# Kernel tuning notes

Measured on AMD Instinct MI355X. Metric: run time of the kernel, lower is better.

The kernel has to match this reference:

```python
import jax, jax.numpy as jnp
import numpy as np

N = 200000
F_IN = 128
F_OUT = 128
NBRS = 4  # NEIGHBORHOOD_SIZE - 1 (self counted separately)


def setup_inputs() -> dict:
    key = jax.random.key(0)
    k1, k2, k3, k4, k5 = jax.random.split(key, 5)
    features = jax.random.normal(k1, (N, F_IN), dtype=jnp.float32)
    prev_features = jax.random.normal(k2, (N, F_IN), dtype=jnp.float32)
    neighbor_idx = jax.random.randint(k3, (N, NBRS), 0, N, dtype=jnp.int32)
    # nn.Linear(5*in, out): weight [out, 5*in], bias [out]
    W = jax.random.normal(k4, (F_OUT, 5 * F_IN), dtype=jnp.float32) * 0.02
    b = jax.random.normal(k5, (F_OUT,), dtype=jnp.float32) * 0.02
    return {"features": features, "prev_features": prev_features,
            "neighbor_idx": neighbor_idx, "W": W, "b": b}


def reference(features, prev_features, neighbor_idx, W, b):
    # gather neighbor prev_features: [N, 4, F_IN] -> [N, 4*F_IN]
    nbr = prev_features[neighbor_idx].reshape(N, NBRS * F_IN)
    # concat self features first (matches torch loop order): [N, 5*F_IN]
    gathered = jnp.concatenate([features, nbr], axis=1)
    # linear: y = gathered @ W^T + b -> [N, F_OUT]
    new_features = jnp.einsum('nk,ok->no', gathered, W) + b
    # module sets tet.features = new_features and prev_features = features;
    # both end up equal to new_features.
    return new_features
```

## Files before the change

kernel.cpp:

```cpp
#include <hip/hip_runtime.h>


#define N_PTS  200000
#define F_INN  128
#define K_TOT  640
#define NCHUNK 40
#define NCT    4

typedef __attribute__((ext_vector_type(8)))  short bf16x8;
typedef __attribute__((ext_vector_type(16))) float f32x16;
typedef __attribute__((ext_vector_type(8)))  float f32x8;

union Frag { bf16x8 v; unsigned int u[4]; };

__device__ __forceinline__ unsigned int bf_rne_bits(float f) {
    unsigned int u = __builtin_bit_cast(unsigned int, f);
    return (u + 0x7FFFu + ((u >> 16) & 1u)) & 0xFFFF0000u;
}

__device__ __forceinline__ void split8_rne(const f32x8 a, bf16x8& hi, bf16x8& lo) {
    Frag H, L;
#pragma unroll
    for (int p = 0; p < 4; ++p) {
        float f0 = a[2 * p], f1 = a[2 * p + 1];
        unsigned int h0 = bf_rne_bits(f0), h1 = bf_rne_bits(f1);
        float r0 = f0 - __builtin_bit_cast(float, h0);
        float r1 = f1 - __builtin_bit_cast(float, h1);
        unsigned int l0 = bf_rne_bits(r0), l1 = bf_rne_bits(r1);
        H.u[p] = (h0 >> 16) | h1;
        L.u[p] = (l0 >> 16) | l1;
    }
    hi = H.v; lo = L.v;
}

__device__ __forceinline__ void split8_trunc(const f32x8 a, bf16x8& hi, bf16x8& lo) {
    Frag H, L;
#pragma unroll
    for (int p = 0; p < 4; ++p) {
        float f0 = a[2 * p], f1 = a[2 * p + 1];
        unsigned int u0 = __builtin_bit_cast(unsigned int, f0);
        unsigned int u1 = __builtin_bit_cast(unsigned int, f1);
        unsigned int h0 = u0 & 0xFFFF0000u, h1 = u1 & 0xFFFF0000u;
        float r0 = f0 - __builtin_bit_cast(float, h0);
        float r1 = f1 - __builtin_bit_cast(float, h1);
        unsigned int l0 = __builtin_bit_cast(unsigned int, r0);
        unsigned int l1 = __builtin_bit_cast(unsigned int, r1);
        H.u[p] = (h0 >> 16) | h1;
        L.u[p] = (l0 >> 16) | (l1 & 0xFFFF0000u);
    }
    hi = H.v; lo = L.v;
}

__global__ void build_wf(const float* __restrict__ W,
                         bf16x8* __restrict__ wf_hi,
                         bf16x8* __restrict__ wf_lo) {
    int tid = blockIdx.x * blockDim.x + threadIdx.x;
    int lane = tid & 63;
    int ct   = (tid >> 6) & 3;
    int t    = tid >> 8;
    if (t >= NCHUNK) return;
    int c = ct * 32 + (lane & 31);
    int k = t * 16 + (lane >> 5) * 8;
    f32x8 w = *(const f32x8*)(W + (size_t)c * K_TOT + k);
    bf16x8 h, l;
    split8_rne(w, h, l);
    wf_hi[tid] = h;
    wf_lo[tid] = l;
}

__global__ __launch_bounds__(256, 2)
void mcconv(const float* __restrict__ feat, const float* __restrict__ prev,
            const int* __restrict__ nbr, const float* __restrict__ bias,
            const bf16x8* __restrict__ wf_hi, const bf16x8* __restrict__ wf_lo,
            float* __restrict__ out) {
    const int lane = threadIdx.x & 63;
    const int wave = threadIdx.x >> 6;
    const int g    = lane >> 5;
    const int r31  = lane & 31;
    const int n0   = blockIdx.x * 256 + wave * 64;

    int nA = n0 + r31;
    int nB = n0 + 32 + r31;
    int nAc = nA < N_PTS ? nA : N_PTS - 1;
    int nBc = nB < N_PTS ? nB : N_PTS - 1;

    const int4 iA = *(const int4*)(nbr + 4 * (size_t)nAc);
    const int4 iB = *(const int4*)(nbr + 4 * (size_t)nBc);

    f32x16 acc[2][NCT];
#pragma unroll
    for (int m = 0; m < 2; ++m)
#pragma unroll
        for (int c = 0; c < NCT; ++c)
#pragma unroll
            for (int i = 0; i < 16; ++i) acc[m][c][i] = 0.0f;

    for (int s = 0; s < 5; ++s) {
        const float* pA;
        const float* pB;
        if (s == 0)      { pA = feat + (size_t)nAc * F_INN;  pB = feat + (size_t)nBc * F_INN; }
        else if (s == 1) { pA = prev + (size_t)iA.x * F_INN; pB = prev + (size_t)iB.x * F_INN; }
        else if (s == 2) { pA = prev + (size_t)iA.y * F_INN; pB = prev + (size_t)iB.y * F_INN; }
        else if (s == 3) { pA = prev + (size_t)iA.z * F_INN; pB = prev + (size_t)iB.z * F_INN; }
        else             { pA = prev + (size_t)iA.w * F_INN; pB = prev + (size_t)iB.w * F_INN; }

#pragma unroll
        for (int cc = 0; cc < 8; ++cc) {
            const int t = s * 8 + cc;
            f32x8 a0 = *(const f32x8*)(pA + cc * 16 + g * 8);
            f32x8 a1 = *(const f32x8*)(pB + cc * 16 + g * 8);

            bf16x8 bh[NCT], bl[NCT];
#pragma unroll
            for (int ct = 0; ct < NCT; ++ct) {
                int fi = (t * 4 + ct) * 64 + lane;
                bh[ct] = wf_hi[fi];
                bl[ct] = wf_lo[fi];
            }

            bf16x8 a0h, a0l, a1h, a1l;
            split8_trunc(a0, a0h, a0l);
            split8_trunc(a1, a1h, a1l);

#pragma unroll
            for (int ct = 0; ct < NCT; ++ct) {
                acc[0][ct] = __builtin_amdgcn_mfma_f32_32x32x16_bf16(a0h, bh[ct], acc[0][ct], 0, 0, 0);
                acc[0][ct] = __builtin_amdgcn_mfma_f32_32x32x16_bf16(a0l, bh[ct], acc[0][ct], 0, 0, 0);
                acc[0][ct] = __builtin_amdgcn_mfma_f32_32x32x16_bf16(a0h, bl[ct], acc[0][ct], 0, 0, 0);
                acc[1][ct] = __builtin_amdgcn_mfma_f32_32x32x16_bf16(a1h, bh[ct], acc[1][ct], 0, 0, 0);
                acc[1][ct] = __builtin_amdgcn_mfma_f32_32x32x16_bf16(a1l, bh[ct], acc[1][ct], 0, 0, 0);
                acc[1][ct] = __builtin_amdgcn_mfma_f32_32x32x16_bf16(a1h, bl[ct], acc[1][ct], 0, 0, 0);
            }
        }
    }

    float bcol[NCT];
#pragma unroll
    for (int ct = 0; ct < NCT; ++ct) bcol[ct] = bias[ct * 32 + r31];

#pragma unroll
    for (int m = 0; m < 2; ++m) {
        const int nbase = n0 + m * 32 + 4 * g;
#pragma unroll
        for (int reg = 0; reg < 16; ++reg) {
            const int row = nbase + (reg & 3) + 8 * (reg >> 2);
            if (row < N_PTS) {
#pragma unroll
                for (int ct = 0; ct < NCT; ++ct)
                    out[(size_t)row * F_INN + ct * 32 + r31] = acc[m][ct][reg] + bcol[ct];
            }
        }
    }
}

extern "C" void kernel_launch(void* const* d_in, const int* in_sizes, int n_in,
                              void* d_out, int out_size, void* d_ws, size_t ws_size,
                              hipStream_t stream) {
    const float* feat = (const float*)d_in[0];
    const float* prev = (const float*)d_in[1];
    const int*   nbr  = (const int*)d_in[2];
    const float* W    = (const float*)d_in[3];
    const float* bias = (const float*)d_in[4];
    float* out = (float*)d_out;

    bf16x8* wf_hi = (bf16x8*)d_ws;
    bf16x8* wf_lo = (bf16x8*)((char*)d_ws + (size_t)NCHUNK * NCT * 64 * sizeof(bf16x8));

    hipLaunchKernelGGL(build_wf, dim3(NCHUNK), dim3(256), 0, stream, W, wf_hi, wf_lo);

    const int grid = (N_PTS + 255) / 256;
    hipLaunchKernelGGL(mcconv, dim3(grid), dim3(256), 0, stream,
                       feat, prev, nbr, bias, wf_hi, wf_lo, out);
}
```

Baseline: 383.9 us.

## Halve rows per wave, prefetch next A fragment, permute K layout, nontemporal stores

Each wave now handles 32 rows instead of 64. This halves the accumulator registers and lets launch bounds rise to 3 blocks per SIMD for more occupancy. The K dimension is permuted so each lane reads contiguous 64-float halves of a row, and the weight fragments are rebuilt to match. The next A vector is software-prefetched across neighbor segments, and output uses nontemporal stores. The trade-off is that each weight fragment load is reused by half as many rows, doubling weight traffic per output row.

```diff
diff --git a/kernel.cpp b/kernel.cpp
--- a/kernel.cpp
+++ b/kernel.cpp
@@ -4,7 +4,6 @@
 #define N_PTS  200000
 #define F_INN  128
 #define K_TOT  640
-#define NCHUNK 40
 #define NCT    4
 
 typedef __attribute__((ext_vector_type(8)))  short bf16x8;
@@ -58,17 +57,19 @@
     int lane = tid & 63;
     int ct   = (tid >> 6) & 3;
     int t    = tid >> 8;
-    if (t >= NCHUNK) return;
-    int c = ct * 32 + (lane & 31);
-    int k = t * 16 + (lane >> 5) * 8;
-    f32x8 w = *(const f32x8*)(W + (size_t)c * K_TOT + k);
+    if (t >= 40) return;
+    int s  = t >> 3, cc = t & 7;
+    int g  = lane >> 5, r31 = lane & 31;
+    int c  = ct * 32 + r31;
+    int kk = s * 128 + g * 64 + cc * 8;
+    f32x8 w = *(const f32x8*)(W + (size_t)c * K_TOT + kk);
     bf16x8 h, l;
     split8_rne(w, h, l);
     wf_hi[tid] = h;
     wf_lo[tid] = l;
 }
 
-__global__ __launch_bounds__(256, 2)
+__global__ __launch_bounds__(256, 3)
 void mcconv(const float* __restrict__ feat, const float* __restrict__ prev,
             const int* __restrict__ nbr, const float* __restrict__ bias,
             const bf16x8* __restrict__ wf_hi, const bf16x8* __restrict__ wf_lo,
@@ -77,39 +78,32 @@
     const int wave = threadIdx.x >> 6;
     const int g    = lane >> 5;
     const int r31  = lane & 31;
-    const int n0   = blockIdx.x * 256 + wave * 64;
+    const int n0   = blockIdx.x * 128 + wave * 32;
 
-    int nA = n0 + r31;
-    int nB = n0 + 32 + r31;
+    int nA  = n0 + r31;
     int nAc = nA < N_PTS ? nA : N_PTS - 1;
-    int nBc = nB < N_PTS ? nB : N_PTS - 1;
+    const int4 iA = *(const int4*)(nbr + 4 * (size_t)nAc);
 
-    const int4 iA = *(const int4*)(nbr + 4 * (size_t)nAc);
-    const int4 iB = *(const int4*)(nbr + 4 * (size_t)nBc);
+    const float* p0 = feat + (size_t)nAc  * F_INN + g * 64;
+    const float* p1 = prev + (size_t)iA.x * F_INN + g * 64;
+    const float* p2 = prev + (size_t)iA.y * F_INN + g * 64;
+    const float* p3 = prev + (size_t)iA.z * F_INN + g * 64;
+    const float* p4 = prev + (size_t)iA.w * F_INN + g * 64;
 
-    f32x16 acc[2][NCT];
+    f32x16 acc[NCT];
 #pragma unroll
-    for (int m = 0; m < 2; ++m)
+    for (int c = 0; c < NCT; ++c)
 #pragma unroll
-        for (int c = 0; c < NCT; ++c)
-#pragma unroll
-            for (int i = 0; i < 16; ++i) acc[m][c][i] = 0.0f;
+        for (int i = 0; i < 16; ++i) acc[c][i] = 0.0f;
 
-    for (int s = 0; s < 5; ++s) {
-        const float* pA;
-        const float* pB;
-        if (s == 0)      { pA = feat + (size_t)nAc * F_INN;  pB = feat + (size_t)nBc * F_INN; }
-        else if (s == 1) { pA = prev + (size_t)iA.x * F_INN; pB = prev + (size_t)iB.x * F_INN; }
-        else if (s == 2) { pA = prev + (size_t)iA.y * F_INN; pB = prev + (size_t)iB.y * F_INN; }
-        else if (s == 3) { pA = prev + (size_t)iA.z * F_INN; pB = prev + (size_t)iB.z * F_INN; }
-        else             { pA = prev + (size_t)iA.w * F_INN; pB = prev + (size_t)iB.w * F_INN; }
+    f32x8 a_cur = *(const f32x8*)p0;
 
+    auto SEG = [&](int sbase, const float* p, const float* pnext) {
 #pragma unroll
         for (int cc = 0; cc < 8; ++cc) {
-            const int t = s * 8 + cc;
-            f32x8 a0 = *(const f32x8*)(pA + cc * 16 + g * 8);
-            f32x8 a1 = *(const f32x8*)(pB + cc * 16 + g * 8);
-
+            const int t = sbase + cc;
+            f32x8 a_next = (cc < 7) ? *(const f32x8*)(p + (cc + 1) * 8)
+                                    : *(const f32x8*)pnext;
             bf16x8 bh[NCT], bl[NCT];
 #pragma unroll
             for (int ct = 0; ct < NCT; ++ct) {
@@ -117,38 +111,36 @@
                 bh[ct] = wf_hi[fi];
                 bl[ct] = wf_lo[fi];
             }
-
-            bf16x8 a0h, a0l, a1h, a1l;
-            split8_trunc(a0, a0h, a0l);
-            split8_trunc(a1, a1h, a1l);
-
+            bf16x8 ah, al;
+            split8_trunc(a_cur, ah, al);
 #pragma unroll
             for (int ct = 0; ct < NCT; ++ct) {
-                acc[0][ct] = __builtin_amdgcn_mfma_f32_32x32x16_bf16(a0h, bh[ct], acc[0][ct], 0, 0, 0);
-                acc[0][ct] = __builtin_amdgcn_mfma_f32_32x32x16_bf16(a0l, bh[ct], acc[0][ct], 0, 0, 0);
-                acc[0][ct] = __builtin_amdgcn_mfma_f32_32x32x16_bf16(a0h, bl[ct], acc[0][ct], 0, 0, 0);
-                acc[1][ct] = __builtin_amdgcn_mfma_f32_32x32x16_bf16(a1h, bh[ct], acc[1][ct], 0, 0, 0);
-                acc[1][ct] = __builtin_amdgcn_mfma_f32_32x32x16_bf16(a1l, bh[ct], acc[1][ct], 0, 0, 0);
-                acc[1][ct] = __builtin_amdgcn_mfma_f32_32x32x16_bf16(a1h, bl[ct], acc[1][ct], 0, 0, 0);
+                acc[ct] = __builtin_amdgcn_mfma_f32_32x32x16_bf16(ah, bh[ct], acc[ct], 0, 0, 0);
+                acc[ct] = __builtin_amdgcn_mfma_f32_32x32x16_bf16(al, bh[ct], acc[ct], 0, 0, 0);
+                acc[ct] = __builtin_amdgcn_mfma_f32_32x32x16_bf16(ah, bl[ct], acc[ct], 0, 0, 0);
             }
+            a_cur = a_next;
         }
-    }
+    };
+
+    SEG(0,  p0, p1);
+    SEG(8,  p1, p2);
+    SEG(16, p2, p3);
+    SEG(24, p3, p4);
+    SEG(32, p4, p4);
 
     float bcol[NCT];
 #pragma unroll
     for (int ct = 0; ct < NCT; ++ct) bcol[ct] = bias[ct * 32 + r31];
 
 #pragma unroll
-    for (int m = 0; m < 2; ++m) {
-        const int nbase = n0 + m * 32 + 4 * g;
+    for (int reg = 0; reg < 16; ++reg) {
+        const int row = n0 + (reg & 3) + 8 * (reg >> 2) + 4 * g;
+        if (row < N_PTS) {
 #pragma unroll
-        for (int reg = 0; reg < 16; ++reg) {
-            const int row = nbase + (reg & 3) + 8 * (reg >> 2);
-            if (row < N_PTS) {
-#pragma unroll
-                for (int ct = 0; ct < NCT; ++ct)
-                    out[(size_t)row * F_INN + ct * 32 + r31] = acc[m][ct][reg] + bcol[ct];
-            }
+            for (int ct = 0; ct < NCT; ++ct)
+                __builtin_nontemporal_store(acc[ct][reg] + bcol[ct],
+                                            out + (size_t)row * F_INN + ct * 32 + r31);
         }
     }
 }
@@ -164,11 +156,11 @@
     float* out = (float*)d_out;
 
     bf16x8* wf_hi = (bf16x8*)d_ws;
-    bf16x8* wf_lo = (bf16x8*)((char*)d_ws + (size_t)NCHUNK * NCT * 64 * sizeof(bf16x8));
+    bf16x8* wf_lo = (bf16x8*)((char*)d_ws + (size_t)40 * NCT * 64 * sizeof(bf16x8));
 
-    hipLaunchKernelGGL(build_wf, dim3(NCHUNK), dim3(256), 0, stream, W, wf_hi, wf_lo);
+    hipLaunchKernelGGL(build_wf, dim3(40), dim3(256), 0, stream, W, wf_hi, wf_lo);
 
-    const int grid = (N_PTS + 255) / 256;
+    const int grid = (N_PTS + 127) / 128;
     hipLaunchKernelGGL(mcconv, dim3(grid), dim3(256), 0, stream,
                        feat, prev, nbr, bias, wf_hi, wf_lo, out);
 }
```

After: 430.2 us. +12.1%, slower.

## Stage split weight fragments into LDS with double-buffered async global_load_lds

Applied to the files above, without the earlier changes.

Weight hi/lo fragments are now interleaved in one workspace buffer. Each block cooperatively streams 32KB phases of them into LDS with global_load_lds, double-buffered, and reads the B operands from LDS instead of having every wave fetch them from global memory. The goal is to cut redundant L1/L2 weight traffic and load latency competing with the feature gathers. In exchange it adds 64KB of LDS per block and a barrier per phase, and it relies on the barrier covering the async copy completion.

```diff
diff --git a/kernel.cpp b/kernel.cpp
--- a/kernel.cpp
+++ b/kernel.cpp
@@ -4,7 +4,6 @@
 #define N_PTS  200000
 #define F_INN  128
 #define K_TOT  640
-#define NCHUNK 40
 #define NCT    4
 
 typedef __attribute__((ext_vector_type(8)))  short bf16x8;
@@ -51,41 +50,50 @@
     hi = H.v; lo = L.v;
 }
 
-__global__ void build_wf(const float* __restrict__ W,
-                         bf16x8* __restrict__ wf_hi,
-                         bf16x8* __restrict__ wf_lo) {
+__global__ void build_wf(const float* __restrict__ W, bf16x8* __restrict__ wfbuf) {
     int tid = blockIdx.x * blockDim.x + threadIdx.x;
     int lane = tid & 63;
     int ct   = (tid >> 6) & 3;
     int t    = tid >> 8;
-    if (t >= NCHUNK) return;
+    if (t >= 40) return;
     int c = ct * 32 + (lane & 31);
     int k = t * 16 + (lane >> 5) * 8;
     f32x8 w = *(const f32x8*)(W + (size_t)c * K_TOT + k);
     bf16x8 h, l;
     split8_rne(w, h, l);
-    wf_hi[tid] = h;
-    wf_lo[tid] = l;
+    wfbuf[((t * 4 + ct) * 2 + 0) * 64 + lane] = h;
+    wfbuf[((t * 4 + ct) * 2 + 1) * 64 + lane] = l;
 }
 
 __global__ __launch_bounds__(256, 2)
 void mcconv(const float* __restrict__ feat, const float* __restrict__ prev,
             const int* __restrict__ nbr, const float* __restrict__ bias,
-            const bf16x8* __restrict__ wf_hi, const bf16x8* __restrict__ wf_lo,
-            float* __restrict__ out) {
+            const char* __restrict__ wfbuf, float* __restrict__ out) {
+    __shared__ char smem[2 * 32768];
+
     const int lane = threadIdx.x & 63;
     const int wave = threadIdx.x >> 6;
     const int g    = lane >> 5;
     const int r31  = lane & 31;
     const int n0   = blockIdx.x * 256 + wave * 64;
 
-    int nA = n0 + r31;
-    int nB = n0 + 32 + r31;
+    int nA  = n0 + r31;
+    int nB  = n0 + 32 + r31;
     int nAc = nA < N_PTS ? nA : N_PTS - 1;
     int nBc = nB < N_PTS ? nB : N_PTS - 1;
-
     const int4 iA = *(const int4*)(nbr + 4 * (size_t)nAc);
     const int4 iB = *(const int4*)(nbr + 4 * (size_t)nBc);
+
+    const float* s0A = feat + (size_t)nAc  * F_INN;
+    const float* s0B = feat + (size_t)nBc  * F_INN;
+    const float* s1A = prev + (size_t)iA.x * F_INN;
+    const float* s1B = prev + (size_t)iB.x * F_INN;
+    const float* s2A = prev + (size_t)iA.y * F_INN;
+    const float* s2B = prev + (size_t)iB.y * F_INN;
+    const float* s3A = prev + (size_t)iA.z * F_INN;
+    const float* s3B = prev + (size_t)iB.z * F_INN;
+    const float* s4A = prev + (size_t)iA.w * F_INN;
+    const float* s4B = prev + (size_t)iB.w * F_INN;
 
     f32x16 acc[2][NCT];
 #pragma unroll
@@ -95,43 +103,56 @@
 #pragma unroll
             for (int i = 0; i < 16; ++i) acc[m][c][i] = 0.0f;
 
-    for (int s = 0; s < 5; ++s) {
-        const float* pA;
-        const float* pB;
-        if (s == 0)      { pA = feat + (size_t)nAc * F_INN;  pB = feat + (size_t)nBc * F_INN; }
-        else if (s == 1) { pA = prev + (size_t)iA.x * F_INN; pB = prev + (size_t)iB.x * F_INN; }
-        else if (s == 2) { pA = prev + (size_t)iA.y * F_INN; pB = prev + (size_t)iB.y * F_INN; }
-        else if (s == 3) { pA = prev + (size_t)iA.z * F_INN; pB = prev + (size_t)iB.z * F_INN; }
-        else             { pA = prev + (size_t)iA.w * F_INN; pB = prev + (size_t)iB.w * F_INN; }
+    auto STAGE = [&](int buf, int phase) {
+        const char* gsrc = wfbuf + (size_t)phase * 32768 + wave * 8192 + lane * 16;
+        char* ldst = smem + buf * 32768 + wave * 8192;
+#pragma unroll
+        for (int i = 0; i < 8; ++i) {
+            __builtin_amdgcn_global_load_lds(
+                (const __attribute__((address_space(1))) unsigned int*)(gsrc + i * 1024),
+                (__attribute__((address_space(3))) unsigned int*)(ldst + i * 1024),
+                16, 0, 0);
+        }
+    };
 
+    STAGE(0, 0);
+    __syncthreads();
+
+    for (int p = 0; p < 10; ++p) {
+        const int cur = p & 1;
+        if (p < 9) STAGE(cur ^ 1, p + 1);
+
+        const int s   = p >> 1;
+        const int cc0 = (p & 1) * 4;
+        const float *pA, *pB;
+        if      (s == 0) { pA = s0A; pB = s0B; }
+        else if (s == 1) { pA = s1A; pB = s1B; }
+        else if (s == 2) { pA = s2A; pB = s2B; }
+        else if (s == 3) { pA = s3A; pB = s3B; }
+        else             { pA = s4A; pB = s4B; }
+
+        const char* fb = smem + cur * 32768;
 #pragma unroll
-        for (int cc = 0; cc < 8; ++cc) {
-            const int t = s * 8 + cc;
-            f32x8 a0 = *(const f32x8*)(pA + cc * 16 + g * 8);
-            f32x8 a1 = *(const f32x8*)(pB + cc * 16 + g * 8);
-
-            bf16x8 bh[NCT], bl[NCT];
+        for (int c = 0; c < 4; ++c) {
+            const int cc = cc0 + c;
+            f32x8 aA = *(const f32x8*)(pA + cc * 16 + g * 8);
+            f32x8 aB = *(const f32x8*)(pB + cc * 16 + g * 8);
+            bf16x8 ahA, alA, ahB, alB;
+            split8_trunc(aA, ahA, alA);
+            split8_trunc(aB, ahB, alB);
 #pragma unroll
             for (int ct = 0; ct < NCT; ++ct) {
-                int fi = (t * 4 + ct) * 64 + lane;
-                bh[ct] = wf_hi[fi];
-                bl[ct] = wf_lo[fi];
-            }
-
-            bf16x8 a0h, a0l, a1h, a1l;
-            split8_trunc(a0, a0h, a0l);
-            split8_trunc(a1, a1h, a1l);
-
-#pragma unroll
-            for (int ct = 0; ct < NCT; ++ct) {
-                acc[0][ct] = __builtin_amdgcn_mfma_f32_32x32x16_bf16(a0h, bh[ct], acc[0][ct], 0, 0, 0);
-                acc[0][ct] = __builtin_amdgcn_mfma_f32_32x32x16_bf16(a0l, bh[ct], acc[0][ct], 0, 0, 0);
-                acc[0][ct] = __builtin_amdgcn_mfma_f32_32x32x16_bf16(a0h, bl[ct], acc[0][ct], 0, 0, 0);
-                acc[1][ct] = __builtin_amdgcn_mfma_f32_32x32x16_bf16(a1h, bh[ct], acc[1][ct], 0, 0, 0);
-                acc[1][ct] = __builtin_amdgcn_mfma_f32_32x32x16_bf16(a1l, bh[ct], acc[1][ct], 0, 0, 0);
-                acc[1][ct] = __builtin_amdgcn_mfma_f32_32x32x16_bf16(a1h, bl[ct], acc[1][ct], 0, 0, 0);
+                bf16x8 bh = *(const bf16x8*)(fb + c * 8192 + ct * 2048 +        lane * 16);
+                bf16x8 bl = *(const bf16x8*)(fb + c * 8192 + ct * 2048 + 1024 + lane * 16);
+                acc[0][ct] = __builtin_amdgcn_mfma_f32_32x32x16_bf16(ahA, bh, acc[0][ct], 0, 0, 0);
+                acc[0][ct] = __builtin_amdgcn_mfma_f32_32x32x16_bf16(alA, bh, acc[0][ct], 0, 0, 0);
+                acc[0][ct] = __builtin_amdgcn_mfma_f32_32x32x16_bf16(ahA, bl, acc[0][ct], 0, 0, 0);
+                acc[1][ct] = __builtin_amdgcn_mfma_f32_32x32x16_bf16(ahB, bh, acc[1][ct], 0, 0, 0);
+                acc[1][ct] = __builtin_amdgcn_mfma_f32_32x32x16_bf16(alB, bh, acc[1][ct], 0, 0, 0);
+                acc[1][ct] = __builtin_amdgcn_mfma_f32_32x32x16_bf16(ahB, bl, acc[1][ct], 0, 0, 0);
             }
         }
+        __syncthreads();
     }
 
     float bcol[NCT];
@@ -163,12 +184,11 @@
     const float* bias = (const float*)d_in[4];
     float* out = (float*)d_out;
 
-    bf16x8* wf_hi = (bf16x8*)d_ws;
-    bf16x8* wf_lo = (bf16x8*)((char*)d_ws + (size_t)NCHUNK * NCT * 64 * sizeof(bf16x8));
+    bf16x8* wfbuf = (bf16x8*)d_ws;
 
-    hipLaunchKernelGGL(build_wf, dim3(NCHUNK), dim3(256), 0, stream, W, wf_hi, wf_lo);
+    hipLaunchKernelGGL(build_wf, dim3(40), dim3(256), 0, stream, W, wfbuf);
 
     const int grid = (N_PTS + 255) / 256;
     hipLaunchKernelGGL(mcconv, dim3(grid), dim3(256), 0, stream,
-                       feat, prev, nbr, bias, wf_hi, wf_lo, out);
+                       feat, prev, nbr, bias, (const char*)wfbuf, out);
 }
```

Result: faster. 338.3 us (-11.9%).
